# Optimization experiments

Hardware: AMD Instinct MI355X
Metric: run time of the kernel (lower is better)

## Reference

```python
import jax, jax.numpy as jnp
import numpy as np
import math

D_MODEL = 1024
N_HEADS = 16
HEAD_DIM = D_MODEL // N_HEADS
THETA = 10000.0


def _rope(x, cos, sin):
    # x: [b, h, s, head_dim]; cos/sin: [s, head_dim//2]
    xe = x[..., 0::2]
    xo = x[..., 1::2]
    re = xe * cos - xo * sin
    ro = xe * sin + xo * cos
    # interleave back to even/odd layout
    return jnp.stack([re, ro], axis=-1).reshape(x.shape)


def setup_inputs() -> dict:
    key = jax.random.key(0)
    k1, k2, k3, k4, k5 = jax.random.split(key, 5)
    std = math.sqrt(2.0 / (D_MODEL + D_MODEL))
    x = jax.random.normal(k1, (2, 2048, D_MODEL), dtype=jnp.float32)
    Wq = jax.random.normal(k2, (D_MODEL, D_MODEL), dtype=jnp.float32) * std
    Wk = jax.random.normal(k3, (D_MODEL, D_MODEL), dtype=jnp.float32) * std
    Wv = jax.random.normal(k4, (D_MODEL, D_MODEL), dtype=jnp.float32) * std
    Wo = jax.random.normal(k5, (D_MODEL, D_MODEL), dtype=jnp.float32) * (std / math.sqrt(2))
    return {"x": x, "Wq": Wq, "Wk": Wk, "Wv": Wv, "Wo": Wo}


def reference(x, Wq, Wk, Wv, Wo):
    b, s, d = x.shape
    h, hd = N_HEADS, HEAD_DIM
    # projections: einsum 'batch seq d_in, d_model d_in -> batch seq d_model' == x @ W.T
    def proj(W):
        y = jnp.einsum('bsd,md->bsm', x, W)
        return y.reshape(b, s, h, hd).transpose(0, 2, 1, 3)  # [b, h, s, hd]
    Q, K, V = proj(Wq), proj(Wk), proj(Wv)
    # RoPE with default positions = arange(seq)
    freqs = 1.0 / (THETA ** (jnp.arange(0, hd, 2, dtype=jnp.float32) / hd))
    angles = jnp.arange(s, dtype=jnp.float32)[:, None] * freqs[None, :]  # [s, hd//2]
    cos, sin = jnp.cos(angles), jnp.sin(angles)
    Q = _rope(Q, cos, sin)
    K = _rope(K, cos, sin)
    # naive causal attention
    scores = jnp.einsum('bhqd,bhkd->bhqk', Q, K) / math.sqrt(hd)
    causal = jnp.tril(jnp.ones((s, s), dtype=bool))
    scores = jnp.where(causal, scores, -jnp.inf)
    attn = jax.nn.softmax(scores, axis=-1)
    out = jnp.einsum('bhqk,bhkd->bhqd', attn, V)
    out = out.transpose(0, 2, 1, 3).reshape(b, s, d)
    return jnp.einsum('bsd,md->bsm', out, Wo)
```

## Files before the change

### kernel.cpp

```cpp
#include <hip/hip_runtime.h>
#include <stdint.h>
#include <stddef.h>

typedef __bf16 bf16;
typedef __bf16 bf16x8 __attribute__((ext_vector_type(8)));
typedef __bf16 bf16x4 __attribute__((ext_vector_type(4)));
typedef short short4v __attribute__((ext_vector_type(4)));
typedef float f32x4 __attribute__((ext_vector_type(4)));

#define GAS __attribute__((address_space(1)))
#define LAS __attribute__((address_space(3)))

__device__ __forceinline__ void async_load16(const void* g, void* l) {
  __builtin_amdgcn_global_load_lds((const GAS void*)g, (LAS void*)l, 16, 0, 0);
}

__device__ __forceinline__ f32x4 mfma16(bf16x4 a, bf16x4 b, f32x4 c) {
#if defined(__HIP_DEVICE_COMPILE__)
#if __has_builtin(__builtin_amdgcn_mfma_f32_16x16x16bf16_1k)
  return __builtin_amdgcn_mfma_f32_16x16x16bf16_1k(
      __builtin_bit_cast(short4v, a), __builtin_bit_cast(short4v, b), c, 0, 0, 0);
#else
  f32x4 d;
  asm volatile("v_mfma_f32_16x16x16_bf16 %0, %1, %2, %3"
               : "=v"(d)
               : "v"(a), "v"(b), "v"(c));
  return d;
#endif
#else
  (void)a; (void)b;
  return c;
#endif
}

__global__ __launch_bounds__(256) void cast_all(
    const float* __restrict__ x, const float* __restrict__ Wq,
    const float* __restrict__ Wk, const float* __restrict__ Wv,
    const float* __restrict__ Wo, bf16* __restrict__ Xh,
    bf16* __restrict__ Wqkv, bf16* __restrict__ Woh) {
  int idx = (blockIdx.x * 256 + threadIdx.x) * 4;
  const float* src;
  bf16* dst;
  float scale = 1.0f;
  if (idx < 4194304) {
    src = x + idx; dst = Xh + idx;
  } else if (idx < 7340032) {
    int j = idx - 4194304;
    if (j < 1048576) {
      src = Wq + j; scale = 0.18033688011112042f;
    } else {
      src = ((j < 2097152) ? Wk : Wv) + (j & 1048575);
    }
    dst = Wqkv + j;
  } else {
    int j = idx - 7340032;
    src = Wo + j; dst = Woh + j;
  }
  float4 v = *(const float4*)src;
  bf16x4 o;
  o[0] = (bf16)(v.x * scale); o[1] = (bf16)(v.y * scale);
  o[2] = (bf16)(v.z * scale); o[3] = (bf16)(v.w * scale);
  *(bf16x4*)dst = o;
}

__global__ __launch_bounds__(256) void gemm_qkv(
    const bf16* __restrict__ A, const bf16* __restrict__ B,
    bf16* __restrict__ QKV2, bf16* __restrict__ Vt, int K) {
  __shared__ __align__(16) bf16 As[128 * 32];
  __shared__ __align__(16) bf16 Bs[128 * 32];
  const int tid = threadIdx.x;
  const int wave = tid >> 6, lane = tid & 63;
  const int bm = blockIdx.y * 128, bn = blockIdx.x * 128;
  const int wm = (wave >> 1) * 64, wn = (wave & 1) * 64;
  const int lrow = lane >> 2, lk = (lane & 3) * 8;
  const int fr = lane & 15, fk = (lane >> 4) * 8;

  f32x4 acc[4][4] = {};

  for (int kt = 0; kt < K; kt += 32) {
    __syncthreads();
#pragma unroll
    for (int c = 0; c < 2; ++c) {
      const int chunk = wave * 2 + c;
      const bf16* ga = A + (size_t)(bm + chunk * 16 + lrow) * K + kt + lk;
      async_load16(ga, (void*)(As + chunk * 512));
      const bf16* gb = B + (size_t)(bn + chunk * 16 + lrow) * K + kt + lk;
      async_load16(gb, (void*)(Bs + chunk * 512));
    }
    __syncthreads();

    bf16x8 af[4], bfr[4];
#pragma unroll
    for (int i = 0; i < 4; ++i)
      af[i] = *(const bf16x8*)&As[(wm + i * 16 + fr) * 32 + fk];
#pragma unroll
    for (int j = 0; j < 4; ++j)
      bfr[j] = *(const bf16x8*)&Bs[(wn + j * 16 + fr) * 32 + fk];
#pragma unroll
    for (int i = 0; i < 4; ++i)
#pragma unroll
      for (int j = 0; j < 4; ++j)
        acc[i][j] =
            __builtin_amdgcn_mfma_f32_16x16x32_bf16(af[i], bfr[j], acc[i][j], 0, 0, 0);
  }

  const int r0 = (lane >> 4) * 4, cc = lane & 15;
#pragma unroll
  for (int i = 0; i < 4; ++i) {
    const int row0 = bm + wm + i * 16 + r0;
#pragma unroll
    for (int j = 0; j < 4; ++j) {
      const int col = bn + wn + j * 16 + cc;
      if (col < 2048) {
#pragma unroll
        for (int r = 0; r < 4; ++r)
          QKV2[(size_t)(row0 + r) * 2048 + col] = (bf16)acc[i][j][r];
      } else {
        const int v = col - 2048, h = v >> 6, d = v & 63;
        const int b = row0 >> 11, s = row0 & 2047;
        bf16x4 o;
#pragma unroll
        for (int r = 0; r < 4; ++r) o[r] = (bf16)acc[i][j][r];
        *(bf16x4*)&Vt[(((size_t)b * 16 + h) * 64 + d) * 2048 + s] = o;
      }
    }
  }
}

template <typename OutT, int BM, int BN>
__global__ __launch_bounds__(256) void gemm_bt(
    const bf16* __restrict__ A, const bf16* __restrict__ B,
    OutT* __restrict__ C, int M, int N, int K) {
  constexpr int ACH = BM / 16, NCH = (BM + BN) / 16, PW = NCH / 4;
  constexpr int FM = BM / 32, FN = BN / 32;
  __shared__ __align__(16) bf16 As[BM * 32];
  __shared__ __align__(16) bf16 Bs[BN * 32];
  const int tid = threadIdx.x;
  const int wave = tid >> 6, lane = tid & 63;
  const int bm = blockIdx.y * BM, bn = blockIdx.x * BN;
  const int wm = (wave >> 1) * (BM / 2), wn = (wave & 1) * (BN / 2);
  const int lrow = lane >> 2, lk = (lane & 3) * 8;
  const int fr = lane & 15, fk = (lane >> 4) * 8;

  f32x4 acc[FM][FN] = {};

  for (int kt = 0; kt < K; kt += 32) {
    __syncthreads();
#pragma unroll
    for (int c = 0; c < PW; ++c) {
      const int chunk = wave * PW + c;
      if (chunk < ACH) {
        const bf16* ga = A + (size_t)(bm + chunk * 16 + lrow) * K + kt + lk;
        async_load16(ga, (void*)(As + chunk * 512));
      } else {
        const int bc = chunk - ACH;
        const bf16* gb = B + (size_t)(bn + bc * 16 + lrow) * K + kt + lk;
        async_load16(gb, (void*)(Bs + bc * 512));
      }
    }
    __syncthreads();

    bf16x8 af[FM], bfr[FN];
#pragma unroll
    for (int i = 0; i < FM; ++i)
      af[i] = *(const bf16x8*)&As[(wm + i * 16 + fr) * 32 + fk];
#pragma unroll
    for (int j = 0; j < FN; ++j)
      bfr[j] = *(const bf16x8*)&Bs[(wn + j * 16 + fr) * 32 + fk];
#pragma unroll
    for (int i = 0; i < FM; ++i)
#pragma unroll
      for (int j = 0; j < FN; ++j)
        acc[i][j] =
            __builtin_amdgcn_mfma_f32_16x16x32_bf16(af[i], bfr[j], acc[i][j], 0, 0, 0);
  }

  const int r0 = (lane >> 4) * 4, cc = lane & 15;
#pragma unroll
  for (int i = 0; i < FM; ++i)
#pragma unroll
    for (int j = 0; j < FN; ++j)
#pragma unroll
      for (int r = 0; r < 4; ++r)
        C[(size_t)(bm + wm + i * 16 + r0 + r) * N + (bn + wn + j * 16 + cc)] =
            (OutT)acc[i][j][r];
}

__global__ __launch_bounds__(256) void rope_qk(const bf16* __restrict__ QKV2,
                                               bf16* __restrict__ Qh,
                                               bf16* __restrict__ Kh) {
  int idx = blockIdx.x * 256 + threadIdx.x;
  int row = idx >> 8, grp = idx & 255;
  int col = grp << 3;
  bf16x8 v = *(const bf16x8*)&QKV2[(size_t)row * 2048 + col];
  int s = row & 2047, b = row >> 11;
  bf16x8 o;
#pragma unroll
  for (int k = 0; k < 4; ++k) {
    int cp = (col >> 1) + k;
    int i = cp & 31;
    float freq = __expf((float)i * -0.2878231366242557f);
    float sn, cs;
    __sincosf((float)s * freq, &sn, &cs);
    float xe = (float)v[2 * k], xo = (float)v[2 * k + 1];
    o[2 * k] = (bf16)(xe * cs - xo * sn);
    o[2 * k + 1] = (bf16)(xe * sn + xo * cs);
  }
  int hcol = col & 1023;
  int h = hcol >> 6, d = hcol & 63;
  bf16* dst = (col < 1024 ? Qh : Kh) + ((size_t)(b * 16 + h) * 2048 + s) * 64 + d;
  *(bf16x8*)dst = o;
}

__global__ __launch_bounds__(128, 2) void attn(const bf16* __restrict__ Qh,
                                               const bf16* __restrict__ Kh,
                                               const bf16* __restrict__ Vt,
                                               bf16* __restrict__ Oh) {
  __shared__ __align__(16) bf16 Vs[2][64 * 72];
  __shared__ float scratch[68 * 64];
  const int f = blockIdx.x;
  const int qt = 31 - (f >> 5);
  const int bh = f & 31;
  const int tid = threadIdx.x, w = tid >> 6, lane = tid & 63;
  const int nlo = lane & 15, g = lane >> 4;
  const int q0 = qt * 64;
  const bf16* __restrict__ Qp = Qh + (size_t)bh * 131072;
  const bf16* __restrict__ Kp = Kh + (size_t)bh * 131072;
  const bf16* __restrict__ Vp = Vt + (size_t)bh * 131072;
  const int n = qt + 1;
  const int hf = (n + 1) >> 1;
  const int t0 = w ? hf : 0;
  const int cnt = w ? (n - hf) : hf;

  bf16x8 aq[4][2];
#pragma unroll
  for (int qb = 0; qb < 4; ++qb)
#pragma unroll
    for (int ks = 0; ks < 2; ++ks)
      aq[qb][ks] =
          *(const bf16x8*)&Qp[(size_t)(q0 + qb * 16 + nlo) * 64 + ks * 32 + g * 8];

  f32x4 oacc[4][4] = {};
  float lsum[4] = {0.f, 0.f, 0.f, 0.f};

  const int srow = lane >> 3, soff = (lane & 7) * 8;
  bf16* __restrict__ Vw = Vs[w];

  bf16x8 pv[8];
  if (cnt > 0) {
#pragma unroll
    for (int c = 0; c < 8; ++c)
      pv[c] = *(const bf16x8*)&Vp[(size_t)(c * 8 + srow) * 2048 + t0 * 64 + soff];
  }

  for (int it = 0; it < cnt; ++it) {
    const int i = t0 + it, kbase = i * 64;
    bf16x8 pk[4][2];
#pragma unroll
    for (int ni = 0; ni < 4; ++ni)
#pragma unroll
      for (int ks = 0; ks < 2; ++ks)
        pk[ni][ks] = *(const bf16x8*)&Kp[(size_t)(kbase + ni * 16 + nlo) * 64 +
                                         ks * 32 + g * 8];
#pragma unroll
    for (int c = 0; c < 8; ++c)
      *(bf16x8*)&Vw[(c * 8 + srow) * 72 + soff] = pv[c];
    if (it + 1 < cnt) {
      const int kb2 = kbase + 64;
#pragma unroll
      for (int c = 0; c < 8; ++c)
        pv[c] = *(const bf16x8*)&Vp[(size_t)(c * 8 + srow) * 2048 + kb2 + soff];
    }

    const bool dg = (i == n - 1);
    bf16x4 p[4][4];
#pragma unroll
    for (int qb = 0; qb < 4; ++qb) {
      f32x4 st[4] = {};
#pragma unroll
      for (int ks = 0; ks < 2; ++ks)
#pragma unroll
        for (int ni = 0; ni < 4; ++ni)
          st[ni] = __builtin_amdgcn_mfma_f32_16x16x32_bf16(pk[ni][ks], aq[qb][ks],
                                                           st[ni], 0, 0, 0);
      const int qg = q0 + qb * 16 + nlo;
#pragma unroll
      for (int ni = 0; ni < 4; ++ni) {
        const int kg0 = kbase + ni * 16 + g * 4;
#pragma unroll
        for (int r = 0; r < 4; ++r) {
          float e = __builtin_amdgcn_exp2f(st[ni][r]);
          e = (!dg || (kg0 + r <= qg)) ? e : 0.0f;
          lsum[qb] += e;
          p[qb][ni][r] = (bf16)e;
        }
      }
    }

#pragma unroll
    for (int ni = 0; ni < 4; ++ni)
#pragma unroll
      for (int mi = 0; mi < 4; ++mi) {
        bf16x4 av = *(const bf16x4*)&Vw[(mi * 16 + nlo) * 72 + ni * 16 + g * 4];
#pragma unroll
        for (int qb = 0; qb < 4; ++qb)
          oacc[qb][mi] = mfma16(av, p[qb][ni], oacc[qb][mi]);
      }
  }

#pragma unroll
  for (int qb = 0; qb < 4; ++qb) {
    lsum[qb] += __shfl_xor(lsum[qb], 16, 64);
    lsum[qb] += __shfl_xor(lsum[qb], 32, 64);
  }

  if (w == 1) {
#pragma unroll
    for (int qb = 0; qb < 4; ++qb) {
#pragma unroll
      for (int mi = 0; mi < 4; ++mi)
#pragma unroll
        for (int r = 0; r < 4; ++r)
          scratch[(qb * 16 + mi * 4 + r) * 64 + lane] = oacc[qb][mi][r];
      scratch[(64 + qb) * 64 + lane] = lsum[qb];
    }
  }
  __syncthreads();
  if (w == 0) {
    const int b = bh >> 4, hd = bh & 15;
#pragma unroll
    for (int qb = 0; qb < 4; ++qb) {
      const float l = lsum[qb] + scratch[(64 + qb) * 64 + lane];
      const float inv = 1.0f / l;
      const int q = q0 + qb * 16 + nlo;
#pragma unroll
      for (int mi = 0; mi < 4; ++mi) {
        bf16x4 o;
#pragma unroll
        for (int r = 0; r < 4; ++r)
          o[r] = (bf16)((oacc[qb][mi][r] +
                         scratch[(qb * 16 + mi * 4 + r) * 64 + lane]) * inv);
        *(bf16x4*)&Oh[((size_t)b * 2048 + q) * 1024 + hd * 64 + mi * 16 + g * 4] = o;
      }
    }
  }
}

extern "C" void kernel_launch(void* const* d_in, const int* in_sizes, int n_in,
                              void* d_out, int out_size, void* d_ws, size_t ws_size,
                              hipStream_t stream) {
  (void)in_sizes; (void)n_in; (void)out_size; (void)ws_size;
  const float* x = (const float*)d_in[0];
  const float* Wq = (const float*)d_in[1];
  const float* Wk = (const float*)d_in[2];
  const float* Wv = (const float*)d_in[3];
  const float* Wo = (const float*)d_in[4];
  float* out = (float*)d_out;
  char* ws = (char*)d_ws;

  bf16* Xh   = (bf16*)(ws);
  bf16* Wqkv = (bf16*)(ws + 8388608);
  bf16* Woh  = (bf16*)(ws + 14680064);
  bf16* QKV2 = (bf16*)(ws + 16777216);
  bf16* Qh   = (bf16*)(ws + 33554432);
  bf16* Kh   = (bf16*)(ws + 41943040);
  bf16* Vt   = (bf16*)(ws + 50331648);
  bf16* Oh   = (bf16*)(ws + 58720256);

  cast_all<<<8192, 256, 0, stream>>>(x, Wq, Wk, Wv, Wo, Xh, Wqkv, Woh);
  gemm_qkv<<<dim3(24, 32), 256, 0, stream>>>(Xh, Wqkv, QKV2, Vt, 1024);
  rope_qk<<<4096, 256, 0, stream>>>(QKV2, Qh, Kh);
  attn<<<1024, 128, 0, stream>>>(Qh, Kh, Vt, Oh);
  gemm_bt<float, 128, 64><<<dim3(16, 32), 256, 0, stream>>>(Oh, Woh, out, 4096, 1024, 1024);
}
```

Before: 196.4 us.

## Fuse RoPE into QKV GEMM epilogue and prefetch K tiles in attention

The separate rope_qk kernel is removed. The QKV GEMM epilogue now applies the rotary embedding itself, using a lane shuffle to fetch the even/odd partner, and writes Q and K straight into head-major layout. This drops the intermediate QKV2 buffer round trip and one kernel launch. In attention, K fragments are now prefetched one iteration ahead like V, and all QK^T MFMAs are issued before the softmax, which gives more overlap at the cost of more registers. The fused epilogue writes scalar bf16 values with a stride of 64 elements, which is less coalesced than the old vector writes.

```diff
diff --git a/kernel.cpp b/kernel.cpp
--- a/kernel.cpp
+++ b/kernel.cpp
@@ -65,7 +65,8 @@
 
 __global__ __launch_bounds__(256) void gemm_qkv(
     const bf16* __restrict__ A, const bf16* __restrict__ B,
-    bf16* __restrict__ QKV2, bf16* __restrict__ Vt, int K) {
+    bf16* __restrict__ Qh, bf16* __restrict__ Kh, bf16* __restrict__ Vt,
+    int K) {
   __shared__ __align__(16) bf16 As[128 * 32];
   __shared__ __align__(16) bf16 Bs[128 * 32];
   const int tid = threadIdx.x;
@@ -105,23 +106,35 @@
   }
 
   const int r0 = (lane >> 4) * 4, cc = lane & 15;
+  const bool oddl = cc & 1;
 #pragma unroll
   for (int i = 0; i < 4; ++i) {
     const int row0 = bm + wm + i * 16 + r0;
+    const int b = row0 >> 11, s0 = row0 & 2047;
 #pragma unroll
     for (int j = 0; j < 4; ++j) {
       const int col = bn + wn + j * 16 + cc;
       if (col < 2048) {
-#pragma unroll
-        for (int r = 0; r < 4; ++r)
-          QKV2[(size_t)(row0 + r) * 2048 + col] = (bf16)acc[i][j][r];
+        const int hcol = col & 1023;
+        const int h = hcol >> 6, d = hcol & 63;
+        const int ip = d >> 1;
+        const float freq = __expf((float)ip * -0.2878231366242557f);
+        bf16* dst = (col < 1024 ? Qh : Kh) + ((size_t)(b * 16 + h) * 2048) * 64 + d;
+#pragma unroll
+        for (int r = 0; r < 4; ++r) {
+          float own = acc[i][j][r];
+          float oth = __shfl_xor(own, 1, 64);
+          float sn, cs;
+          __sincosf((float)(s0 + r) * freq, &sn, &cs);
+          float res = oddl ? (oth * sn + own * cs) : (own * cs - oth * sn);
+          dst[(size_t)(s0 + r) * 64] = (bf16)res;
+        }
       } else {
         const int v = col - 2048, h = v >> 6, d = v & 63;
-        const int b = row0 >> 11, s = row0 & 2047;
         bf16x4 o;
 #pragma unroll
         for (int r = 0; r < 4; ++r) o[r] = (bf16)acc[i][j][r];
-        *(bf16x4*)&Vt[(((size_t)b * 16 + h) * 64 + d) * 2048 + s] = o;
+        *(bf16x4*)&Vt[(((size_t)b * 16 + h) * 64 + d) * 2048 + s0] = o;
       }
     }
   }
@@ -184,32 +197,6 @@
       for (int r = 0; r < 4; ++r)
         C[(size_t)(bm + wm + i * 16 + r0 + r) * N + (bn + wn + j * 16 + cc)] =
             (OutT)acc[i][j][r];
-}
-
-__global__ __launch_bounds__(256) void rope_qk(const bf16* __restrict__ QKV2,
-                                               bf16* __restrict__ Qh,
-                                               bf16* __restrict__ Kh) {
-  int idx = blockIdx.x * 256 + threadIdx.x;
-  int row = idx >> 8, grp = idx & 255;
-  int col = grp << 3;
-  bf16x8 v = *(const bf16x8*)&QKV2[(size_t)row * 2048 + col];
-  int s = row & 2047, b = row >> 11;
-  bf16x8 o;
-#pragma unroll
-  for (int k = 0; k < 4; ++k) {
-    int cp = (col >> 1) + k;
-    int i = cp & 31;
-    float freq = __expf((float)i * -0.2878231366242557f);
-    float sn, cs;
-    __sincosf((float)s * freq, &sn, &cs);
-    float xe = (float)v[2 * k], xo = (float)v[2 * k + 1];
-    o[2 * k] = (bf16)(xe * cs - xo * sn);
-    o[2 * k + 1] = (bf16)(xe * sn + xo * cs);
-  }
-  int hcol = col & 1023;
-  int h = hcol >> 6, d = hcol & 63;
-  bf16* dst = (col < 1024 ? Qh : Kh) + ((size_t)(b * 16 + h) * 2048 + s) * 64 + d;
-  *(bf16x8*)dst = o;
 }
 
 __global__ __launch_bounds__(128, 2) void attn(const bf16* __restrict__ Qh,
@@ -246,28 +233,49 @@
   const int srow = lane >> 3, soff = (lane & 7) * 8;
   bf16* __restrict__ Vw = Vs[w];
 
-  bf16x8 pv[8];
+  bf16x8 pv[8], pk[4][2];
   if (cnt > 0) {
 #pragma unroll
     for (int c = 0; c < 8; ++c)
       pv[c] = *(const bf16x8*)&Vp[(size_t)(c * 8 + srow) * 2048 + t0 * 64 + soff];
+#pragma unroll
+    for (int ni = 0; ni < 4; ++ni)
+#pragma unroll
+      for (int ks = 0; ks < 2; ++ks)
+        pk[ni][ks] = *(const bf16x8*)&Kp[(size_t)(t0 * 64 + ni * 16 + nlo) * 64 +
+                                         ks * 32 + g * 8];
   }
 
   for (int it = 0; it < cnt; ++it) {
     const int i = t0 + it, kbase = i * 64;
-    bf16x8 pk[4][2];
-#pragma unroll
-    for (int ni = 0; ni < 4; ++ni)
-#pragma unroll
-      for (int ks = 0; ks < 2; ++ks)
-        pk[ni][ks] = *(const bf16x8*)&Kp[(size_t)(kbase + ni * 16 + nlo) * 64 +
-                                         ks * 32 + g * 8];
 #pragma unroll
     for (int c = 0; c < 8; ++c)
       *(bf16x8*)&Vw[(c * 8 + srow) * 72 + soff] = pv[c];
+
+    f32x4 st[4][4];
+#pragma unroll
+    for (int qb = 0; qb < 4; ++qb)
+#pragma unroll
+      for (int ni = 0; ni < 4; ++ni)
+        st[qb][ni] = (f32x4){0.f, 0.f, 0.f, 0.f};
+#pragma unroll
+    for (int ks = 0; ks < 2; ++ks)
+#pragma unroll
+      for (int ni = 0; ni < 4; ++ni)
+#pragma unroll
+        for (int qb = 0; qb < 4; ++qb)
+          st[qb][ni] = __builtin_amdgcn_mfma_f32_16x16x32_bf16(
+              pk[ni][ks], aq[qb][ks], st[qb][ni], 0, 0, 0);
+
     if (it + 1 < cnt) {
       const int kb2 = kbase + 64;
 #pragma unroll
+      for (int ni = 0; ni < 4; ++ni)
+#pragma unroll
+        for (int ks = 0; ks < 2; ++ks)
+          pk[ni][ks] = *(const bf16x8*)&Kp[(size_t)(kb2 + ni * 16 + nlo) * 64 +
+                                           ks * 32 + g * 8];
+#pragma unroll
       for (int c = 0; c < 8; ++c)
         pv[c] = *(const bf16x8*)&Vp[(size_t)(c * 8 + srow) * 2048 + kb2 + soff];
     }
@@ -276,20 +284,13 @@
     bf16x4 p[4][4];
 #pragma unroll
     for (int qb = 0; qb < 4; ++qb) {
-      f32x4 st[4] = {};
-#pragma unroll
-      for (int ks = 0; ks < 2; ++ks)
-#pragma unroll
-        for (int ni = 0; ni < 4; ++ni)
-          st[ni] = __builtin_amdgcn_mfma_f32_16x16x32_bf16(pk[ni][ks], aq[qb][ks],
-                                                           st[ni], 0, 0, 0);
       const int qg = q0 + qb * 16 + nlo;
 #pragma unroll
       for (int ni = 0; ni < 4; ++ni) {
         const int kg0 = kbase + ni * 16 + g * 4;
 #pragma unroll
         for (int r = 0; r < 4; ++r) {
-          float e = __builtin_amdgcn_exp2f(st[ni][r]);
+          float e = __builtin_amdgcn_exp2f(st[qb][ni][r]);
           e = (!dg || (kg0 + r <= qg)) ? e : 0.0f;
           lsum[qb] += e;
           p[qb][ni][r] = (bf16)e;
@@ -361,15 +362,13 @@
   bf16* Xh   = (bf16*)(ws);
   bf16* Wqkv = (bf16*)(ws + 8388608);
   bf16* Woh  = (bf16*)(ws + 14680064);
-  bf16* QKV2 = (bf16*)(ws + 16777216);
-  bf16* Qh   = (bf16*)(ws + 33554432);
-  bf16* Kh   = (bf16*)(ws + 41943040);
-  bf16* Vt   = (bf16*)(ws + 50331648);
-  bf16* Oh   = (bf16*)(ws + 58720256);
+  bf16* Qh   = (bf16*)(ws + 16777216);
+  bf16* Kh   = (bf16*)(ws + 25165824);
+  bf16* Vt   = (bf16*)(ws + 33554432);
+  bf16* Oh   = (bf16*)(ws + 41943040);
 
   cast_all<<<8192, 256, 0, stream>>>(x, Wq, Wk, Wv, Wo, Xh, Wqkv, Woh);
-  gemm_qkv<<<dim3(24, 32), 256, 0, stream>>>(Xh, Wqkv, QKV2, Vt, 1024);
-  rope_qk<<<4096, 256, 0, stream>>>(QKV2, Qh, Kh);
+  gemm_qkv<<<dim3(24, 32), 256, 0, stream>>>(Xh, Wqkv, Qh, Kh, Vt, 1024);
   attn<<<1024, 128, 0, stream>>>(Qh, Kh, Vt, Oh);
   gemm_bt<float, 128, 64><<<dim3(16, 32), 256, 0, stream>>>(Oh, Woh, out, 4096, 1024, 1024);
 }
```

After: 218.2 us. +11.1%, slower.
